# Kernel tuning notes

Measured on AMD Instinct MI355X. Metric: run time of the kernel, lower is better.

The kernel has to match this reference:

```python
import jax, jax.numpy as jnp
import numpy as np

N = 50000          # nodes
E_RAND = 800000    # random edges (self-loops appended -> total 850000)
F_IN = 256         # features_num
H = 128            # hidden
HEADS = 4          # headslayers
C = 40             # num_class
OUTDIM = H + HEADS * H + H  # 768, cat of [x_lin, conv1, conv2]
LRELU = 0.01       # F.leaky_relu default slope
ATT_SLOPE = 0.2    # PyG GATConv negative_slope
BN_EPS = 1e-5


def setup_inputs() -> dict:
    key = jax.random.key(0)
    ks = jax.random.split(key, 20)
    src = jax.random.randint(ks[0], (E_RAND,), 0, N)
    dst = jax.random.randint(ks[1], (E_RAND,), 0, N)
    loops = jnp.arange(N, dtype=src.dtype)
    edge_index = jnp.stack([jnp.concatenate([src, loops]),
                            jnp.concatenate([dst, loops])], axis=0)
    g = lambda k, shape, fan: jax.random.normal(k, shape, jnp.float32) * (1.0 / np.sqrt(fan))
    return {
        "x": jax.random.normal(ks[2], (N, F_IN), jnp.float32),
        "edge_index": edge_index,
        # first_lin
        "fw_W": g(ks[3], (F_IN, H), F_IN), "fw_b": jnp.zeros((H,), jnp.float32),
        # conv1: GATConv(H, H, heads=HEADS)
        "c1_W": g(ks[4], (H, HEADS * H), H),
        "c1_as": g(ks[5], (HEADS, H), H), "c1_ad": g(ks[6], (HEADS, H), H),
        "c1_b": jnp.zeros((HEADS * H,), jnp.float32),
        # conv2: GATConv(HEADS*H, H, heads=1)
        "c2_W": g(ks[7], (HEADS * H, H), HEADS * H),
        "c2_as": g(ks[8], (1, H), H), "c2_ad": g(ks[9], (1, H), H),
        "c2_b": jnp.zeros((H,), jnp.float32),
        # batchnorms (training-mode batch stats)
        "bn1_g": jnp.ones((H,), jnp.float32), "bn1_b": jnp.zeros((H,), jnp.float32),
        "bn2_g": jnp.ones((HEADS * H,), jnp.float32), "bn2_b": jnp.zeros((HEADS * H,), jnp.float32),
        "bn3_g": jnp.ones((H,), jnp.float32), "bn3_b": jnp.zeros((H,), jnp.float32),
        # lin2
        "l2_W": g(ks[10], (OUTDIM, C), OUTDIM), "l2_b": jnp.zeros((C,), jnp.float32),
    }


def _batchnorm(x, gamma, beta):
    mu = jnp.mean(x, axis=0)
    var = jnp.mean(jnp.square(x - mu), axis=0)  # biased, as torch BN training
    return (x - mu) * (gamma / jnp.sqrt(var + BN_EPS)) + beta


def _gat_conv(x, edge_index, W, a_src, a_dst, bias, heads, out_dim):
    src, dst = edge_index[0], edge_index[1]
    h = (x @ W).reshape(-1, heads, out_dim)            # [N, heads, out]
    alpha_s = jnp.sum(h * a_src, axis=-1)              # [N, heads]
    alpha_d = jnp.sum(h * a_dst, axis=-1)              # [N, heads]
    e = alpha_s[src] + alpha_d[dst]                    # [E, heads]
    e = jnp.where(e >= 0, e, ATT_SLOPE * e)            # leaky_relu(0.2)
    # segment softmax over incoming edges of each dst node
    emax = jax.ops.segment_max(e, dst, num_segments=N)
    e = jnp.exp(e - emax[dst])
    denom = jax.ops.segment_sum(e, dst, num_segments=N)
    alpha = e / (denom[dst] + 1e-16)                   # [E, heads]
    msg = h[src] * alpha[:, :, None]                   # [E, heads, out]
    out = jax.ops.segment_sum(msg, dst, num_segments=N)
    return out.reshape(-1, heads * out_dim) + bias


def _lrelu(x):
    return jnp.where(x >= 0, x, LRELU * x)


def reference(x, edge_index, fw_W, fw_b, c1_W, c1_as, c1_ad, c1_b,
              c2_W, c2_as, c2_ad, c2_b, bn1_g, bn1_b, bn2_g, bn2_b,
              bn3_g, bn3_b, l2_W, l2_b):
    h = _lrelu(x @ fw_W + fw_b)
    h = _batchnorm(h, bn1_g, bn1_b)
    feats = [h]
    h = _lrelu(_gat_conv(h, edge_index, c1_W, c1_as, c1_ad, c1_b, HEADS, H))
    h = _batchnorm(h, bn2_g, bn2_b)
    feats.append(h)
    h = _lrelu(_gat_conv(h, edge_index, c2_W, c2_as, c2_ad, c2_b, 1, H))
    h = _batchnorm(h, bn3_g, bn3_b)
    feats.append(h)
    z = jnp.concatenate(feats, axis=1) @ l2_W + l2_b
    return jax.nn.log_softmax(z, axis=-1)
```

## Files before the change

kernel.cpp:

```cpp
#include <hip/hip_runtime.h>

#define INF_F __builtin_inff()

typedef unsigned short u16;
typedef __attribute__((ext_vector_type(8))) short s16x8;
typedef __attribute__((ext_vector_type(4))) float f32x4;

union U8 { uint4 q; s16x8 v; };

__device__ __forceinline__ float b2f(u16 u) {
    union { unsigned int i; float f; } v; v.i = ((unsigned int)u) << 16; return v.f;
}
__device__ __forceinline__ u16 f2b(float f) {
    union { float f; unsigned int i; } v; v.f = f;
    unsigned int r = (v.i + 0x7FFFu + ((v.i >> 16) & 1u)) >> 16;
    return (u16)r;
}
__device__ __forceinline__ void bf2x(unsigned int p, float& lo, float& hi) {
    union { unsigned int i; float f; } a, b;
    a.i = p << 16; b.i = p & 0xFFFF0000u;
    lo = a.f; hi = b.f;
}
__device__ __forceinline__ unsigned int packbf(float lo, float hi) {
    return (unsigned int)f2b(lo) | ((unsigned int)f2b(hi) << 16);
}

__device__ __forceinline__ void pack_one(const float* __restrict__ W, int K, int N,
                                         int Npad, u16* __restrict__ pb, int idx)
{
    int k = idx / Npad, n = idx - k * Npad;
    float v = (n < N) ? W[(size_t)k * N + n] : 0.f;
    int K5 = K >> 5;
    size_t o = ((size_t)(n >> 4) * K5 + (k >> 5)) * 512
             + ((size_t)((k >> 3) & 3)) * 128 + (n & 15) * 8 + (k & 7);
    pb[o] = f2b(v);
}

__launch_bounds__(256)
__global__ void k_prep(const float* __restrict__ fw_W, const float* __restrict__ c1_W,
                       const float* __restrict__ c2_W, const float* __restrict__ l2_W,
                       u16* __restrict__ pb_l1, u16* __restrict__ pb_c1,
                       u16* __restrict__ pb_c2, u16* __restrict__ pb_f,
                       const int* __restrict__ dst, int E, int* __restrict__ counts)
{
    int idx = blockIdx.x * 256 + threadIdx.x;
    if (idx < 32768) { pack_one(fw_W, 256, 128, 128, pb_l1, idx); return; }
    idx -= 32768;
    if (idx < 65536) { pack_one(c1_W, 128, 512, 512, pb_c1, idx); return; }
    idx -= 65536;
    if (idx < 65536) { pack_one(c2_W, 512, 128, 128, pb_c2, idx); return; }
    idx -= 65536;
    if (idx < 49152) { pack_one(l2_W, 768, 40, 64, pb_f, idx); return; }
    idx -= 49152;
    if (idx < E) atomicAdd(&counts[dst[idx]], 1);
}

__launch_bounds__(256)
__global__ void k_l1sc(const float* __restrict__ x, const u16* __restrict__ pb,
                       u16* __restrict__ h1, int M, const float* __restrict__ bias,
                       int mb2, const int* __restrict__ ei, int E,
                       const int* __restrict__ rowstart, int* __restrict__ fill,
                       int* __restrict__ csr)
{
    if ((int)blockIdx.x >= mb2) {
        int e = ((int)blockIdx.x - mb2) * 256 + threadIdx.x;
        if (e < E) {
            int s = ei[e], d = ei[E + e];
            int pos = rowstart[d] + atomicAdd(&fill[d], 1);
            csr[pos] = s;
        }
        return;
    }
    const int tid = threadIdx.x;
    const int w = tid >> 6, l = tid & 63;
    const int lo = l & 15, hi = l >> 4;
    const int row0 = blockIdx.x * 128 + w * 32;
    if (row0 >= M) return;

    f32x4 acc[8][2];
    #pragma unroll
    for (int i = 0; i < 8; ++i)
        #pragma unroll
        for (int s = 0; s < 2; ++s) acc[i][s] = (f32x4){0.f, 0.f, 0.f, 0.f};

    int arow[2];
    #pragma unroll
    for (int s = 0; s < 2; ++s) {
        int r = row0 + s * 16 + lo;
        arow[s] = r < M ? r : M - 1;
    }

    for (int k5 = 0; k5 < 8; ++k5) {
        const int ak = k5 * 32 + hi * 8;
        s16x8 af[2];
        #pragma unroll
        for (int s = 0; s < 2; ++s) {
            const float* A = x + (size_t)arow[s] * 256 + ak;
            float4 v0 = *reinterpret_cast<const float4*>(A);
            float4 v1 = *reinterpret_cast<const float4*>(A + 4);
            U8 au;
            au.q.x = packbf(v0.x, v0.y); au.q.y = packbf(v0.z, v0.w);
            au.q.z = packbf(v1.x, v1.y); au.q.w = packbf(v1.z, v1.w);
            af[s] = au.v;
        }
        #pragma unroll
        for (int cb = 0; cb < 8; ++cb) {
            s16x8 bf = *reinterpret_cast<const s16x8*>(pb + ((size_t)cb * 8 + k5) * 512 + l * 8);
            acc[cb][0] = __builtin_amdgcn_mfma_f32_16x16x32_bf16(af[0], bf, acc[cb][0], 0, 0, 0);
            acc[cb][1] = __builtin_amdgcn_mfma_f32_16x16x32_bf16(af[1], bf, acc[cb][1], 0, 0, 0);
        }
    }

    #pragma unroll
    for (int cb = 0; cb < 8; ++cb) {
        int col = cb * 16 + lo;
        #pragma unroll
        for (int s = 0; s < 2; ++s) {
            #pragma unroll
            for (int p = 0; p < 4; ++p) {
                int r = row0 + s * 16 + hi * 4 + p;
                if (r < M) {
                    float v = acc[cb][s][p] + bias[col];
                    v = v >= 0.f ? v : 0.01f * v;
                    h1[(size_t)r * 128 + col] = f2b(v);
                }
            }
        }
    }
}

template<int NFRAG, bool BN_A, int HEADS_PB>
__launch_bounds__(256)
__global__ void k_mgemm(const u16* __restrict__ Av, int lda, int K,
                        const u16* __restrict__ pb,
                        u16* __restrict__ C, int ldc, int M,
                        const float* __restrict__ scale, const float* __restrict__ shift,
                        const float* __restrict__ aw_s, const float* __restrict__ aw_d,
                        float* __restrict__ as_o, float* __restrict__ ad_o, int nheads)
{
    const int tid = threadIdx.x;
    const int w = tid >> 6, l = tid & 63;
    const int lo = l & 15, hi = l >> 4;
    const int row0 = blockIdx.y * 128 + w * 32;
    if (row0 >= M) return;
    const int cb0 = blockIdx.x * NFRAG;
    const int K5 = K >> 5;

    f32x4 acc[NFRAG][2];
    #pragma unroll
    for (int i = 0; i < NFRAG; ++i)
        #pragma unroll
        for (int s = 0; s < 2; ++s) acc[i][s] = (f32x4){0.f, 0.f, 0.f, 0.f};

    int arow[2];
    #pragma unroll
    for (int s = 0; s < 2; ++s) {
        int r = row0 + s * 16 + lo;
        arow[s] = r < M ? r : M - 1;
    }

    for (int k5 = 0; k5 < K5; ++k5) {
        const int ak = k5 * 32 + hi * 8;
        s16x8 af[2];
        #pragma unroll
        for (int s = 0; s < 2; ++s) {
            uint4 q = *reinterpret_cast<const uint4*>(Av + (size_t)arow[s] * lda + ak);
            float x[8];
            bf2x(q.x, x[0], x[1]); bf2x(q.y, x[2], x[3]);
            bf2x(q.z, x[4], x[5]); bf2x(q.w, x[6], x[7]);
            if (BN_A) {
                #pragma unroll
                for (int j = 0; j < 8; ++j) x[j] = fmaf(x[j], scale[ak + j], shift[ak + j]);
            }
            U8 au;
            au.q.x = packbf(x[0], x[1]); au.q.y = packbf(x[2], x[3]);
            au.q.z = packbf(x[4], x[5]); au.q.w = packbf(x[6], x[7]);
            af[s] = au.v;
        }
        #pragma unroll
        for (int cb = 0; cb < NFRAG; ++cb) {
            s16x8 bf = *reinterpret_cast<const s16x8*>(
                pb + ((size_t)(cb0 + cb) * K5 + k5) * 512 + l * 8);
            acc[cb][0] = __builtin_amdgcn_mfma_f32_16x16x32_bf16(af[0], bf, acc[cb][0], 0, 0, 0);
            acc[cb][1] = __builtin_amdgcn_mfma_f32_16x16x32_bf16(af[1], bf, acc[cb][1], 0, 0, 0);
        }
    }

    #pragma unroll
    for (int cb = 0; cb < NFRAG; ++cb) {
        int col = (cb0 + cb) * 16 + lo;
        #pragma unroll
        for (int s = 0; s < 2; ++s) {
            #pragma unroll
            for (int p = 0; p < 4; ++p) {
                int r = row0 + s * 16 + hi * 4 + p;
                if (r < M) C[(size_t)r * ldc + col] = f2b(acc[cb][s][p]);
            }
        }
    }

    if (HEADS_PB > 0) {
        const int h = (cb0 >> 3);
        #pragma unroll
        for (int s = 0; s < 2; ++s) {
            float ps[4] = {0.f,0.f,0.f,0.f}, pd[4] = {0.f,0.f,0.f,0.f};
            #pragma unroll
            for (int cb = 0; cb < NFRAG; ++cb) {
                int col = (cb0 + cb) * 16 + lo;
                float ws = aw_s[col], wd = aw_d[col];
                #pragma unroll
                for (int p = 0; p < 4; ++p) {
                    ps[p] = fmaf(acc[cb][s][p], ws, ps[p]);
                    pd[p] = fmaf(acc[cb][s][p], wd, pd[p]);
                }
            }
            #pragma unroll
            for (int m = 1; m < 16; m <<= 1) {
                #pragma unroll
                for (int p = 0; p < 4; ++p) {
                    ps[p] += __shfl_xor(ps[p], m, 64);
                    pd[p] += __shfl_xor(pd[p], m, 64);
                }
            }
            if (lo == 0) {
                #pragma unroll
                for (int p = 0; p < 4; ++p) {
                    int r = row0 + s * 16 + hi * 4 + p;
                    if (r < M) {
                        as_o[(size_t)r * nheads + h] = ps[p];
                        ad_o[(size_t)r * nheads + h] = pd[p];
                    }
                }
            }
        }
    }
}

__launch_bounds__(256)
__global__ void k_mfinal(const u16* __restrict__ h1, const u16* __restrict__ h2,
                         const u16* __restrict__ h3,
                         const float* __restrict__ scale, const float* __restrict__ shift,
                         const u16* __restrict__ pb, const float* __restrict__ bias,
                         float* __restrict__ out, int M)
{
    const int tid = threadIdx.x;
    const int w = tid >> 6, l = tid & 63;
    const int lo = l & 15, hi = l >> 4;
    const int row0 = blockIdx.x * 128 + w * 32;
    if (row0 >= M) return;
    const int K5 = 24;

    f32x4 acc[4][2];
    #pragma unroll
    for (int i = 0; i < 4; ++i)
        #pragma unroll
        for (int s = 0; s < 2; ++s) acc[i][s] = (f32x4){0.f, 0.f, 0.f, 0.f};

    int arow[2];
    #pragma unroll
    for (int s = 0; s < 2; ++s) {
        int r = row0 + s * 16 + lo;
        arow[s] = r < M ? r : M - 1;
    }

    for (int k5 = 0; k5 < K5; ++k5) {
        const int kk = k5 * 32 + hi * 8;
        const u16* src; int ld, offk;
        if (kk < 128)      { src = h1; ld = 128; offk = kk; }
        else if (kk < 640) { src = h2; ld = 512; offk = kk - 128; }
        else               { src = h3; ld = 128; offk = kk - 640; }
        s16x8 af[2];
        #pragma unroll
        for (int s = 0; s < 2; ++s) {
            uint4 q = *reinterpret_cast<const uint4*>(src + (size_t)arow[s] * ld + offk);
            float x[8];
            bf2x(q.x, x[0], x[1]); bf2x(q.y, x[2], x[3]);
            bf2x(q.z, x[4], x[5]); bf2x(q.w, x[6], x[7]);
            #pragma unroll
            for (int j = 0; j < 8; ++j) x[j] = fmaf(x[j], scale[kk + j], shift[kk + j]);
            U8 au;
            au.q.x = packbf(x[0], x[1]); au.q.y = packbf(x[2], x[3]);
            au.q.z = packbf(x[4], x[5]); au.q.w = packbf(x[6], x[7]);
            af[s] = au.v;
        }
        #pragma unroll
        for (int cb = 0; cb < 4; ++cb) {
            s16x8 bf = *reinterpret_cast<const s16x8*>(pb + ((size_t)cb * K5 + k5) * 512 + l * 8);
            acc[cb][0] = __builtin_amdgcn_mfma_f32_16x16x32_bf16(af[0], bf, acc[cb][0], 0, 0, 0);
            acc[cb][1] = __builtin_amdgcn_mfma_f32_16x16x32_bf16(af[1], bf, acc[cb][1], 0, 0, 0);
        }
    }

    #pragma unroll
    for (int s = 0; s < 2; ++s) {
        #pragma unroll
        for (int p = 0; p < 4; ++p) {
            int r = row0 + s * 16 + hi * 4 + p;
            float z0 = acc[0][s][p] + bias[lo];
            float z1 = acc[1][s][p] + bias[16 + lo];
            float z2 = -INF_F;
            if (lo < 8) z2 = acc[2][s][p] + bias[32 + lo];
            float mx = fmaxf(fmaxf(z0, z1), z2);
            #pragma unroll
            for (int m = 1; m < 16; m <<= 1) mx = fmaxf(mx, __shfl_xor(mx, m, 64));
            float se = __expf(z0 - mx) + __expf(z1 - mx) + ((lo < 8) ? __expf(z2 - mx) : 0.f);
            #pragma unroll
            for (int m = 1; m < 16; m <<= 1) se += __shfl_xor(se, m, 64);
            float lse = mx + __logf(se);
            if (r < M) {
                out[(size_t)r * 40 + lo]      = z0 - lse;
                out[(size_t)r * 40 + 16 + lo] = z1 - lse;
                if (lo < 8) out[(size_t)r * 40 + 32 + lo] = z2 - lse;
            }
        }
    }
}

__launch_bounds__(256)
__global__ void k_colstats(const u16* __restrict__ X, int M, int C,
                           float* __restrict__ psum, float* __restrict__ psq)
{
    const int CG  = C >> 3;
    const int RPI = 256 / CG;
    const int tid = threadIdx.x;
    const int cg  = tid & (CG - 1);
    const int ro  = tid / CG;
    const int nb  = gridDim.x;
    const int rows_chunk = (M + nb - 1) / nb;
    const int r0 = blockIdx.x * rows_chunk;
    const int r1 = min(M, r0 + rows_chunk);

    float s[8] = {}, q[8] = {};
    for (int r = r0 + ro; r < r1; r += RPI) {
        uint4 u = *reinterpret_cast<const uint4*>(X + (size_t)r * C + cg * 8);
        float x[8];
        bf2x(u.x, x[0], x[1]); bf2x(u.y, x[2], x[3]);
        bf2x(u.z, x[4], x[5]); bf2x(u.w, x[6], x[7]);
        #pragma unroll
        for (int j = 0; j < 8; ++j) { s[j] += x[j]; q[j] = fmaf(x[j], x[j], q[j]); }
    }

    __shared__ float lsum[8][256];
    __shared__ float lsq [8][256];
    #pragma unroll
    for (int j = 0; j < 8; ++j) { lsum[j][tid] = s[j]; lsq[j][tid] = q[j]; }
    __syncthreads();

    if (tid < CG) {
        #pragma unroll
        for (int j = 0; j < 8; ++j) {
            float ss = 0.f, qq = 0.f;
            for (int o = 0; o < RPI; ++o) {
                ss += lsum[j][o * CG + tid];
                qq += lsq [j][o * CG + tid];
            }
            psum[(size_t)blockIdx.x * C + tid * 8 + j] = ss;
            psq [(size_t)blockIdx.x * C + tid * 8 + j] = qq;
        }
    }
}

__launch_bounds__(256)
__global__ void k_colred(const float* __restrict__ psum, const float* __restrict__ psq,
                         const float* __restrict__ g, const float* __restrict__ b,
                         int nb, int M, int C,
                         float* __restrict__ scale, float* __restrict__ shift)
{
    int c = blockIdx.x * 4 + (threadIdx.x >> 6);
    int lane = threadIdx.x & 63;
    if (c >= C) return;
    float s = 0.f, q = 0.f;
    for (int l = lane; l < nb; l += 64) {
        s += psum[(size_t)l * C + c];
        q += psq [(size_t)l * C + c];
    }
    #pragma unroll
    for (int off = 32; off; off >>= 1) {
        s += __shfl_xor(s, off, 64);
        q += __shfl_xor(q, off, 64);
    }
    if (lane == 0) {
        float mu  = s / (float)M;
        float var = q / (float)M - mu * mu;
        float sc  = g[c] * rsqrtf(var + 1e-5f);
        scale[c] = sc;
        shift[c] = b[c] - mu * sc;
    }
}

__launch_bounds__(256)
__global__ void k_scan1(const int* __restrict__ counts, int n,
                        int* __restrict__ rowstart, int* __restrict__ tilesum,
                        int* __restrict__ fill)
{
    const int tid = threadIdx.x;
    const int lane = tid & 63, w = tid >> 6;
    const int i0 = blockIdx.x * 1024 + tid * 4;
    int v0 = 0, v1 = 0, v2 = 0, v3 = 0;
    if (i0 + 3 < n) {
        int4 q = *reinterpret_cast<const int4*>(counts + i0);
        v0 = q.x; v1 = q.y; v2 = q.z; v3 = q.w;
    } else if (i0 < n) {
        v0 = counts[i0];
        if (i0 + 1 < n) v1 = counts[i0 + 1];
        if (i0 + 2 < n) v2 = counts[i0 + 2];
    }
    if (i0 < n) {
        int4 z = make_int4(0, 0, 0, 0);
        if (i0 + 3 < n) *reinterpret_cast<int4*>(fill + i0) = z;
        else {
            fill[i0] = 0;
            if (i0 + 1 < n) fill[i0 + 1] = 0;
            if (i0 + 2 < n) fill[i0 + 2] = 0;
        }
    }
    int s1 = v0 + v1, s2 = s1 + v2, s3 = s2 + v3;
    int x = s3;
    #pragma unroll
    for (int off = 1; off < 64; off <<= 1) {
        int t = __shfl_up(x, off, 64);
        if (lane >= off) x += t;
    }
    __shared__ int wsum[4];
    if (lane == 63) wsum[w] = x;
    __syncthreads();
    int woff = 0;
    #pragma unroll
    for (int i = 0; i < 4; ++i)
        if (i < w) woff += wsum[i];
    int excl = woff + x - s3;
    if (i0 + 0 < n) rowstart[i0 + 1] = excl + v0;
    if (i0 + 1 < n) rowstart[i0 + 2] = excl + s1;
    if (i0 + 2 < n) rowstart[i0 + 3] = excl + s2;
    if (i0 + 3 < n) rowstart[i0 + 4] = excl + s3;
    if (tid == 255) tilesum[blockIdx.x] = wsum[0] + wsum[1] + wsum[2] + wsum[3];
}

__launch_bounds__(256)
__global__ void k_scan3(int* __restrict__ rowstart, const int* __restrict__ tilesum, int n)
{
    const int tile = (int)((blockIdx.x * 256) >> 10);
    __shared__ int s_off;
    if (threadIdx.x < 64) {
        int lane = threadIdx.x;
        int v = (lane < tile) ? tilesum[lane] : 0;
        #pragma unroll
        for (int m = 1; m < 64; m <<= 1) v += __shfl_xor(v, m, 64);
        if (lane == 0) s_off = v;
    }
    __syncthreads();
    int i = blockIdx.x * 256 + threadIdx.x;
    if (i < n) rowstart[i + 1] += s_off;
    if (blockIdx.x == 0 && threadIdx.x == 0) rowstart[0] = 0;
}

__launch_bounds__(256)
__global__ void k_gat_agg_h4(const u16* __restrict__ hp,
                             const float* __restrict__ as_, const float* __restrict__ ad_,
                             const int* __restrict__ rowstart, const int* __restrict__ csr,
                             const float* __restrict__ bias, u16* __restrict__ out, int Nn)
{
    int d = (int)((blockIdx.x * (size_t)blockDim.x + threadIdx.x) >> 6);
    int lane = threadIdx.x & 63;
    if (d >= Nn) return;
    const int h = lane >> 4;
    const int li = lane & 15;
    const int dim = li * 8;
    int e0 = rowstart[d], e1 = rowstart[d + 1];
    float adv = ad_[(size_t)d * 4 + h];

    float mx = -INF_F;
    for (int j = e0 + li; j < e1; j += 16) {
        int s = csr[j];
        float e = as_[(size_t)s * 4 + h] + adv;
        e = e >= 0.f ? e : 0.2f * e;
        mx = fmaxf(mx, e);
    }
    #pragma unroll
    for (int m = 1; m < 16; m <<= 1) mx = fmaxf(mx, __shfl_xor(mx, m, 64));

    float lsum = 0.f;
    float acc[8] = {};

    #define F4(J, A, U) { int jj = min((J), e1 - 1); int s_ = csr[jj];                \
        A = as_[(size_t)s_ * 4 + h];                                                  \
        U = *reinterpret_cast<const uint4*>(hp + ((size_t)s_ * 4 + h) * 128 + dim); }
    #define C4(A, U) { float e_ = A + adv; e_ = e_ >= 0.f ? e_ : 0.2f * e_;           \
        float w_ = __expf(e_ - mx); lsum += w_;                                       \
        float x_[8];                                                                  \
        bf2x(U.x, x_[0], x_[1]); bf2x(U.y, x_[2], x_[3]);                             \
        bf2x(U.z, x_[4], x_[5]); bf2x(U.w, x_[6], x_[7]);                             \
        _Pragma("unroll")                                                             \
        for (int t_ = 0; t_ < 8; ++t_) acc[t_] = fmaf(x_[t_], w_, acc[t_]); }

    float a0, a1, a2, a3, a4, a5, a6, a7;
    uint4 u0, u1, u2, u3, u4, u5, u6, u7;
    F4(e0 + 0, a0, u0); F4(e0 + 1, a1, u1); F4(e0 + 2, a2, u2); F4(e0 + 3, a3, u3);
    F4(e0 + 4, a4, u4); F4(e0 + 5, a5, u5); F4(e0 + 6, a6, u6); F4(e0 + 7, a7, u7);

    int j = e0;
    for (; j + 3 < e1; j += 4) {
        C4(a0, u0); C4(a1, u1); C4(a2, u2); C4(a3, u3);
        a0 = a4; u0 = u4; a1 = a5; u1 = u5; a2 = a6; u2 = u6; a3 = a7; u3 = u7;
        F4(j + 8, a4, u4); F4(j + 9, a5, u5); F4(j + 10, a6, u6); F4(j + 11, a7, u7);
    }
    if (j < e1)     C4(a0, u0);
    if (j + 1 < e1) C4(a1, u1);
    if (j + 2 < e1) C4(a2, u2);
    #undef F4
    #undef C4

    float inv = 1.f / (lsum + 1e-16f);
    const int ob = h * 128 + dim;
    float v[8];
    #pragma unroll
    for (int t = 0; t < 8; ++t) {
        float z = acc[t] * inv + bias[ob + t];
        v[t] = z >= 0.f ? z : 0.01f * z;
    }
    uint4 o;
    o.x = packbf(v[0], v[1]); o.y = packbf(v[2], v[3]);
    o.z = packbf(v[4], v[5]); o.w = packbf(v[6], v[7]);
    *reinterpret_cast<uint4*>(out + (size_t)d * 512 + ob) = o;
}

__launch_bounds__(256)
__global__ void k_gat_agg_h1(const u16* __restrict__ hp,
                             const float* __restrict__ as_, const float* __restrict__ ad_,
                             const int* __restrict__ rowstart, const int* __restrict__ csr,
                             const float* __restrict__ bias, u16* __restrict__ out, int Nn)
{
    const int lane = threadIdx.x & 63;
    const int half = lane >> 5;
    const int sl = lane & 31;
    const int wave = (int)((blockIdx.x * (size_t)blockDim.x + threadIdx.x) >> 6);
    const int d = wave * 2 + half;
    if (wave * 2 >= Nn) return;
    const bool act = d < Nn;
    const int dc = act ? d : (Nn - 1);
    const int dim = sl * 4;
    int e0 = rowstart[dc], e1 = rowstart[dc + 1];
    int len = e1 - e0;
    float adv = ad_[dc];

    float mx = -INF_F;
    for (int j = e0 + sl; j < e1; j += 32) {
        int s = csr[j];
        float e = as_[s] + adv;
        e = e >= 0.f ? e : 0.2f * e;
        mx = fmaxf(mx, e);
    }
    #pragma unroll
    for (int m = 1; m < 32; m <<= 1) mx = fmaxf(mx, __shfl_xor(mx, m, 32));

    int maxlen = max(len, __shfl_xor(len, 32, 64));

    float lsum = 0.f;
    float acc[4] = {};

    #define F1(JR, A, U) { int jj = e0 + min((JR), len - 1); int s_ = csr[jj];        \
        A = as_[s_];                                                                  \
        U = *reinterpret_cast<const uint2*>(hp + (size_t)s_ * 128 + dim); }
    #define C1(JR, A, U) { float e_ = A + adv; e_ = e_ >= 0.f ? e_ : 0.2f * e_;       \
        float w_ = ((JR) < len) ? __expf(e_ - mx) : 0.f;                              \
        float x0_, x1_, x2_, x3_; bf2x(U.x, x0_, x1_); bf2x(U.y, x2_, x3_);           \
        lsum += w_;                                                                   \
        acc[0] = fmaf(x0_, w_, acc[0]); acc[1] = fmaf(x1_, w_, acc[1]);               \
        acc[2] = fmaf(x2_, w_, acc[2]); acc[3] = fmaf(x3_, w_, acc[3]); }

    float a0, a1, a2, a3, a4, a5, a6, a7;
    uint2 u0, u1, u2, u3, u4, u5, u6, u7;
    F1(0, a0, u0); F1(1, a1, u1); F1(2, a2, u2); F1(3, a3, u3);
    F1(4, a4, u4); F1(5, a5, u5); F1(6, a6, u6); F1(7, a7, u7);

    int jr = 0;
    for (; jr + 3 < maxlen; jr += 4) {
        C1(jr + 0, a0, u0); C1(jr + 1, a1, u1); C1(jr + 2, a2, u2); C1(jr + 3, a3, u3);
        a0 = a4; u0 = u4; a1 = a5; u1 = u5; a2 = a6; u2 = u6; a3 = a7; u3 = u7;
        F1(jr + 8, a4, u4); F1(jr + 9, a5, u5); F1(jr + 10, a6, u6); F1(jr + 11, a7, u7);
    }
    if (jr < maxlen)     C1(jr + 0, a0, u0);
    if (jr + 1 < maxlen) C1(jr + 1, a1, u1);
    if (jr + 2 < maxlen) C1(jr + 2, a2, u2);
    #undef F1
    #undef C1

    float inv = 1.f / (lsum + 1e-16f);
    float v0 = acc[0] * inv + bias[dim];
    float v1 = acc[1] * inv + bias[dim + 1];
    float v2 = acc[2] * inv + bias[dim + 2];
    float v3 = acc[3] * inv + bias[dim + 3];
    v0 = v0 >= 0.f ? v0 : 0.01f * v0;
    v1 = v1 >= 0.f ? v1 : 0.01f * v1;
    v2 = v2 >= 0.f ? v2 : 0.01f * v2;
    v3 = v3 >= 0.f ? v3 : 0.01f * v3;
    if (act) {
        uint2 o;
        o.x = packbf(v0, v1);
        o.y = packbf(v2, v3);
        *reinterpret_cast<uint2*>(out + (size_t)d * 128 + dim) = o;
    }
}

extern "C" void kernel_launch(void* const* d_in, const int* in_sizes, int n_in,
                              void* d_out, int out_size, void* d_ws, size_t ws_size,
                              hipStream_t stream)
{
    const float* x     = (const float*)d_in[0];
    const int*   ei    = (const int*)  d_in[1];
    const float* fw_W  = (const float*)d_in[2];
    const float* fw_b  = (const float*)d_in[3];
    const float* c1_W  = (const float*)d_in[4];
    const float* c1_as = (const float*)d_in[5];
    const float* c1_ad = (const float*)d_in[6];
    const float* c1_b  = (const float*)d_in[7];
    const float* c2_W  = (const float*)d_in[8];
    const float* c2_as = (const float*)d_in[9];
    const float* c2_ad = (const float*)d_in[10];
    const float* c2_b  = (const float*)d_in[11];
    const float* bn1_g = (const float*)d_in[12];
    const float* bn1_b = (const float*)d_in[13];
    const float* bn2_g = (const float*)d_in[14];
    const float* bn2_b = (const float*)d_in[15];
    const float* bn3_g = (const float*)d_in[16];
    const float* bn3_b = (const float*)d_in[17];
    const float* l2_W  = (const float*)d_in[18];
    const float* l2_b  = (const float*)d_in[19];
    float* out = (float*)d_out;

    const int N = in_sizes[0] / 256;
    const int E = in_sizes[1] / 2;
    const int NB = 256;

    char* base = (char*)d_ws;
    size_t off = 0;
    auto alloc = [&](size_t bytes) -> void* {
        void* p = (void*)(base + off);
        off = (off + bytes + 255) & ~(size_t)255;
        return p;
    };
    int*   counts = (int*)  alloc((size_t)N * 4);
    size_t zero_bytes = off;
    const int SCB = (N + 1023) / 1024;
    int*   fill     = (int*)  alloc((size_t)N * 4);
    float* as1      = (float*)alloc((size_t)N * 4 * 4);
    float* ad1      = (float*)alloc((size_t)N * 4 * 4);
    float* as2      = (float*)alloc((size_t)N * 4);
    float* ad2      = (float*)alloc((size_t)N * 4);
    float* psum     = (float*)alloc((size_t)NB * 512 * 4);
    float* psq      = (float*)alloc((size_t)NB * 512 * 4);
    int*   rowstart = (int*)  alloc((size_t)(N + 1) * 4);
    int*   tilesum  = (int*)  alloc((size_t)SCB * 4);
    int*   csr      = (int*)  alloc((size_t)E * 4);
    float* scale768 = (float*)alloc(768 * 4);
    float* shift768 = (float*)alloc(768 * 4);
    u16*   pb_l1    = (u16*)  alloc((size_t)256 * 128 * 2);
    u16*   pb_c1    = (u16*)  alloc((size_t)128 * 512 * 2);
    u16*   pb_c2    = (u16*)  alloc((size_t)512 * 128 * 2);
    u16*   pb_f     = (u16*)  alloc((size_t)768 * 64 * 2);
    u16*   h1       = (u16*)  alloc((size_t)N * 128 * 2);
    u16*   h2       = (u16*)  alloc((size_t)N * 512 * 2);
    u16*   hp1      = (u16*)  alloc((size_t)N * 512 * 2);
    u16*   hp2      = hp1;
    u16*   h3       = hp1 + (size_t)N * 128;
    (void)ws_size; (void)n_in; (void)out_size;

    const int mb2 = (N + 127) / 128;
    const int scb = (E + 255) / 256;
    const int wave_blocks = (int)(((size_t)N * 64 + 255) / 256);
    const int h1_wave_blocks = (int)((((size_t)N + 1) / 2 * 64 + 255) / 256);
    const int PK = 32768 + 65536 + 65536 + 49152;

    hipMemsetAsync(base, 0, zero_bytes, stream);

    k_prep<<<(PK + E + 255) / 256, 256, 0, stream>>>(
        fw_W, c1_W, c2_W, l2_W, pb_l1, pb_c1, pb_c2, pb_f, ei + E, E, counts);

    k_scan1<<<SCB, 256, 0, stream>>>(counts, N, rowstart, tilesum, fill);
    k_scan3<<<(N + 255) / 256, 256, 0, stream>>>(rowstart, tilesum, N);

    k_l1sc<<<mb2 + scb, 256, 0, stream>>>(
        x, pb_l1, h1, N, fw_b, mb2, ei, E, rowstart, fill, csr);

    k_colstats<<<NB, 256, 0, stream>>>(h1, N, 128, psum, psq);
    k_colred<<<(128 + 3) / 4, 256, 0, stream>>>(psum, psq, bn1_g, bn1_b, NB, N, 128,
                                                scale768, shift768);

    k_mgemm<8, true, 1><<<dim3(4, mb2), 256, 0, stream>>>(
        h1, 128, 128, pb_c1, hp1, 512, N, scale768, shift768,
        c1_as, c1_ad, as1, ad1, 4);
    k_gat_agg_h4<<<wave_blocks, 256, 0, stream>>>(
        hp1, as1, ad1, rowstart, csr, c1_b, h2, N);

    k_colstats<<<NB, 256, 0, stream>>>(h2, N, 512, psum, psq);
    k_colred<<<(512 + 3) / 4, 256, 0, stream>>>(psum, psq, bn2_g, bn2_b, NB, N, 512,
                                                scale768 + 128, shift768 + 128);

    k_mgemm<8, true, 1><<<dim3(1, mb2), 256, 0, stream>>>(
        h2, 512, 512, pb_c2, hp2, 128, N, scale768 + 128, shift768 + 128,
        c2_as, c2_ad, as2, ad2, 1);
    k_gat_agg_h1<<<h1_wave_blocks, 256, 0, stream>>>(
        hp2, as2, ad2, rowstart, csr, c2_b, h3, N);

    k_colstats<<<NB, 256, 0, stream>>>(h3, N, 128, psum, psq);
    k_colred<<<(128 + 3) / 4, 256, 0, stream>>>(psum, psq, bn3_g, bn3_b, NB, N, 128,
                                                scale768 + 640, shift768 + 640);

    k_mfinal<<<mb2, 256, 0, stream>>>(h1, h2, h3, scale768, shift768, pb_f, l2_b, out, N);
}
```

Baseline: 412.0 us.

## Merge CSR build stages with layer-1 GEMM and BN stats into shared launches

Rearranges the front of the pipeline so independent work shares a launch. The first-layer GEMM runs alongside scan1, scan3 alongside the BN1 column stats, and the edge scatter alongside the BN1 column reduction. This cuts the launch count from five to three and overlaps small latency-bound kernels with bigger ones. The scatter also now handles four edges per thread with int4 loads. The risk is that heterogeneous blocks in one grid may load-balance poorly, and the larger shared-memory footprint of the combined kernels can lower occupancy.

```diff
diff --git a/kernel.cpp b/kernel.cpp
--- a/kernel.cpp
+++ b/kernel.cpp
@@ -55,26 +55,14 @@
     if (idx < E) atomicAdd(&counts[dst[idx]], 1);
 }
 
-__launch_bounds__(256)
-__global__ void k_l1sc(const float* __restrict__ x, const u16* __restrict__ pb,
-                       u16* __restrict__ h1, int M, const float* __restrict__ bias,
-                       int mb2, const int* __restrict__ ei, int E,
-                       const int* __restrict__ rowstart, int* __restrict__ fill,
-                       int* __restrict__ csr)
-{
-    if ((int)blockIdx.x >= mb2) {
-        int e = ((int)blockIdx.x - mb2) * 256 + threadIdx.x;
-        if (e < E) {
-            int s = ei[e], d = ei[E + e];
-            int pos = rowstart[d] + atomicAdd(&fill[d], 1);
-            csr[pos] = s;
-        }
-        return;
-    }
+__device__ void dev_l1gemm(const float* __restrict__ x, const u16* __restrict__ pb,
+                           u16* __restrict__ h1, int M, const float* __restrict__ bias,
+                           int bid)
+{
     const int tid = threadIdx.x;
     const int w = tid >> 6, l = tid & 63;
     const int lo = l & 15, hi = l >> 4;
-    const int row0 = blockIdx.x * 128 + w * 32;
+    const int row0 = bid * 128 + w * 32;
     if (row0 >= M) return;
 
     f32x4 acc[8][2];
@@ -127,6 +115,210 @@
             }
         }
     }
+}
+
+__device__ void dev_scan1(const int* __restrict__ counts, int n,
+                          int* __restrict__ rowstart, int* __restrict__ tilesum,
+                          int* __restrict__ fill, int bid)
+{
+    const int tid = threadIdx.x;
+    const int lane = tid & 63, w = tid >> 6;
+    const int i0 = bid * 1024 + tid * 4;
+    int v0 = 0, v1 = 0, v2 = 0, v3 = 0;
+    if (i0 + 3 < n) {
+        int4 q = *reinterpret_cast<const int4*>(counts + i0);
+        v0 = q.x; v1 = q.y; v2 = q.z; v3 = q.w;
+    } else if (i0 < n) {
+        v0 = counts[i0];
+        if (i0 + 1 < n) v1 = counts[i0 + 1];
+        if (i0 + 2 < n) v2 = counts[i0 + 2];
+    }
+    if (i0 < n) {
+        int4 z = make_int4(0, 0, 0, 0);
+        if (i0 + 3 < n) *reinterpret_cast<int4*>(fill + i0) = z;
+        else {
+            fill[i0] = 0;
+            if (i0 + 1 < n) fill[i0 + 1] = 0;
+            if (i0 + 2 < n) fill[i0 + 2] = 0;
+        }
+    }
+    int s1 = v0 + v1, s2 = s1 + v2, s3 = s2 + v3;
+    int x = s3;
+    #pragma unroll
+    for (int off = 1; off < 64; off <<= 1) {
+        int t = __shfl_up(x, off, 64);
+        if (lane >= off) x += t;
+    }
+    __shared__ int wsum[4];
+    if (lane == 63) wsum[w] = x;
+    __syncthreads();
+    int woff = 0;
+    #pragma unroll
+    for (int i = 0; i < 4; ++i)
+        if (i < w) woff += wsum[i];
+    int excl = woff + x - s3;
+    if (i0 + 0 < n) rowstart[i0 + 1] = excl + v0;
+    if (i0 + 1 < n) rowstart[i0 + 2] = excl + s1;
+    if (i0 + 2 < n) rowstart[i0 + 3] = excl + s2;
+    if (i0 + 3 < n) rowstart[i0 + 4] = excl + s3;
+    if (tid == 255) tilesum[bid] = wsum[0] + wsum[1] + wsum[2] + wsum[3];
+}
+
+__device__ void dev_scan3(int* __restrict__ rowstart, const int* __restrict__ tilesum,
+                          int n, int bid)
+{
+    const int tile = (bid * 256) >> 10;
+    __shared__ int s_off;
+    if (threadIdx.x < 64) {
+        int lane = threadIdx.x;
+        int v = (lane < tile) ? tilesum[lane] : 0;
+        #pragma unroll
+        for (int m = 1; m < 64; m <<= 1) v += __shfl_xor(v, m, 64);
+        if (lane == 0) s_off = v;
+    }
+    __syncthreads();
+    int i = bid * 256 + threadIdx.x;
+    if (i < n) rowstart[i + 1] += s_off;
+    if (bid == 0 && threadIdx.x == 0) rowstart[0] = 0;
+}
+
+__device__ void dev_colstats(const u16* __restrict__ X, int M, int C,
+                             float* __restrict__ psum, float* __restrict__ psq,
+                             int bid, int nb)
+{
+    const int CG  = C >> 3;
+    const int RPI = 256 / CG;
+    const int tid = threadIdx.x;
+    const int cg  = tid & (CG - 1);
+    const int ro  = tid / CG;
+    const int rows_chunk = (M + nb - 1) / nb;
+    const int r0 = bid * rows_chunk;
+    const int r1 = min(M, r0 + rows_chunk);
+
+    float s[8] = {}, q[8] = {};
+    for (int r = r0 + ro; r < r1; r += RPI) {
+        uint4 u = *reinterpret_cast<const uint4*>(X + (size_t)r * C + cg * 8);
+        float x[8];
+        bf2x(u.x, x[0], x[1]); bf2x(u.y, x[2], x[3]);
+        bf2x(u.z, x[4], x[5]); bf2x(u.w, x[6], x[7]);
+        #pragma unroll
+        for (int j = 0; j < 8; ++j) { s[j] += x[j]; q[j] = fmaf(x[j], x[j], q[j]); }
+    }
+
+    __shared__ float lsum[8][256];
+    __shared__ float lsq [8][256];
+    #pragma unroll
+    for (int j = 0; j < 8; ++j) { lsum[j][tid] = s[j]; lsq[j][tid] = q[j]; }
+    __syncthreads();
+
+    if (tid < CG) {
+        #pragma unroll
+        for (int j = 0; j < 8; ++j) {
+            float ss = 0.f, qq = 0.f;
+            for (int o = 0; o < RPI; ++o) {
+                ss += lsum[j][o * CG + tid];
+                qq += lsq [j][o * CG + tid];
+            }
+            psum[(size_t)bid * C + tid * 8 + j] = ss;
+            psq [(size_t)bid * C + tid * 8 + j] = qq;
+        }
+    }
+}
+
+__device__ void dev_colred(const float* __restrict__ psum, const float* __restrict__ psq,
+                           const float* __restrict__ g, const float* __restrict__ b,
+                           int nb, int M, int C,
+                           float* __restrict__ scale, float* __restrict__ shift, int bid)
+{
+    int c = bid * 4 + ((int)threadIdx.x >> 6);
+    int lane = threadIdx.x & 63;
+    if (c >= C) return;
+    float s = 0.f, q = 0.f;
+    for (int l = lane; l < nb; l += 64) {
+        s += psum[(size_t)l * C + c];
+        q += psq [(size_t)l * C + c];
+    }
+    #pragma unroll
+    for (int off = 32; off; off >>= 1) {
+        s += __shfl_xor(s, off, 64);
+        q += __shfl_xor(q, off, 64);
+    }
+    if (lane == 0) {
+        float mu  = s / (float)M;
+        float var = q / (float)M - mu * mu;
+        float sc  = g[c] * rsqrtf(var + 1e-5f);
+        scale[c] = sc;
+        shift[c] = b[c] - mu * sc;
+    }
+}
+
+__device__ void dev_scatter4(const int* __restrict__ ei, int E,
+                             const int* __restrict__ rowstart,
+                             int* __restrict__ fill, int* __restrict__ csr, int bid)
+{
+    int e0 = (bid * 256 + (int)threadIdx.x) * 4;
+    if (e0 >= E) return;
+    if (e0 + 3 < E) {
+        int4 s4 = *reinterpret_cast<const int4*>(ei + e0);
+        int4 d4 = *reinterpret_cast<const int4*>(ei + E + e0);
+        int p0 = rowstart[d4.x] + atomicAdd(&fill[d4.x], 1); csr[p0] = s4.x;
+        int p1 = rowstart[d4.y] + atomicAdd(&fill[d4.y], 1); csr[p1] = s4.y;
+        int p2 = rowstart[d4.z] + atomicAdd(&fill[d4.z], 1); csr[p2] = s4.z;
+        int p3 = rowstart[d4.w] + atomicAdd(&fill[d4.w], 1); csr[p3] = s4.w;
+    } else {
+        for (int e = e0; e < E; ++e) {
+            int s = ei[e], d = ei[E + e];
+            int pos = rowstart[d] + atomicAdd(&fill[d], 1);
+            csr[pos] = s;
+        }
+    }
+}
+
+__launch_bounds__(256)
+__global__ void kA(const float* __restrict__ x, const u16* __restrict__ pb_l1,
+                   u16* __restrict__ h1, int M, const float* __restrict__ fw_b, int mb2,
+                   const int* __restrict__ counts, int n,
+                   int* __restrict__ rowstart, int* __restrict__ tilesum,
+                   int* __restrict__ fill)
+{
+    if ((int)blockIdx.x < mb2) dev_l1gemm(x, pb_l1, h1, M, fw_b, blockIdx.x);
+    else                       dev_scan1(counts, n, rowstart, tilesum, fill, blockIdx.x - mb2);
+}
+
+__launch_bounds__(256)
+__global__ void kB(int* __restrict__ rowstart, const int* __restrict__ tilesum, int n,
+                   int nscan3, const u16* __restrict__ h1, int M,
+                   float* __restrict__ psum, float* __restrict__ psq, int nb)
+{
+    if ((int)blockIdx.x < nscan3) dev_scan3(rowstart, tilesum, n, blockIdx.x);
+    else                          dev_colstats(h1, M, 128, psum, psq, blockIdx.x - nscan3, nb);
+}
+
+__launch_bounds__(256)
+__global__ void kC(const int* __restrict__ ei, int E, const int* __restrict__ rowstart,
+                   int* __restrict__ fill, int* __restrict__ csr, int nscat,
+                   const float* __restrict__ psum, const float* __restrict__ psq,
+                   const float* __restrict__ g, const float* __restrict__ b,
+                   int nb, int M, float* __restrict__ scale, float* __restrict__ shift)
+{
+    if ((int)blockIdx.x < nscat) dev_scatter4(ei, E, rowstart, fill, csr, blockIdx.x);
+    else dev_colred(psum, psq, g, b, nb, M, 128, scale, shift, blockIdx.x - nscat);
+}
+
+__launch_bounds__(256)
+__global__ void k_colstats(const u16* __restrict__ X, int M, int C,
+                           float* __restrict__ psum, float* __restrict__ psq)
+{
+    dev_colstats(X, M, C, psum, psq, blockIdx.x, gridDim.x);
+}
+
+__launch_bounds__(256)
+__global__ void k_colred(const float* __restrict__ psum, const float* __restrict__ psq,
+                         const float* __restrict__ g, const float* __restrict__ b,
+                         int nb, int M, int C,
+                         float* __restrict__ scale, float* __restrict__ shift)
+{
+    dev_colred(psum, psq, g, b, nb, M, C, scale, shift, blockIdx.x);
 }
 
 template<int NFRAG, bool BN_A, int HEADS_PB>
@@ -314,144 +506,6 @@
             }
         }
     }
-}
-
-__launch_bounds__(256)
-__global__ void k_colstats(const u16* __restrict__ X, int M, int C,
-                           float* __restrict__ psum, float* __restrict__ psq)
-{
-    const int CG  = C >> 3;
-    const int RPI = 256 / CG;
-    const int tid = threadIdx.x;
-    const int cg  = tid & (CG - 1);
-    const int ro  = tid / CG;
-    const int nb  = gridDim.x;
-    const int rows_chunk = (M + nb - 1) / nb;
-    const int r0 = blockIdx.x * rows_chunk;
-    const int r1 = min(M, r0 + rows_chunk);
-
-    float s[8] = {}, q[8] = {};
-    for (int r = r0 + ro; r < r1; r += RPI) {
-        uint4 u = *reinterpret_cast<const uint4*>(X + (size_t)r * C + cg * 8);
-        float x[8];
-        bf2x(u.x, x[0], x[1]); bf2x(u.y, x[2], x[3]);
-        bf2x(u.z, x[4], x[5]); bf2x(u.w, x[6], x[7]);
-        #pragma unroll
-        for (int j = 0; j < 8; ++j) { s[j] += x[j]; q[j] = fmaf(x[j], x[j], q[j]); }
-    }
-
-    __shared__ float lsum[8][256];
-    __shared__ float lsq [8][256];
-    #pragma unroll
-    for (int j = 0; j < 8; ++j) { lsum[j][tid] = s[j]; lsq[j][tid] = q[j]; }
-    __syncthreads();
-
-    if (tid < CG) {
-        #pragma unroll
-        for (int j = 0; j < 8; ++j) {
-            float ss = 0.f, qq = 0.f;
-            for (int o = 0; o < RPI; ++o) {
-                ss += lsum[j][o * CG + tid];
-                qq += lsq [j][o * CG + tid];
-            }
-            psum[(size_t)blockIdx.x * C + tid * 8 + j] = ss;
-            psq [(size_t)blockIdx.x * C + tid * 8 + j] = qq;
-        }
-    }
-}
-
-__launch_bounds__(256)
-__global__ void k_colred(const float* __restrict__ psum, const float* __restrict__ psq,
-                         const float* __restrict__ g, const float* __restrict__ b,
-                         int nb, int M, int C,
-                         float* __restrict__ scale, float* __restrict__ shift)
-{
-    int c = blockIdx.x * 4 + (threadIdx.x >> 6);
-    int lane = threadIdx.x & 63;
-    if (c >= C) return;
-    float s = 0.f, q = 0.f;
-    for (int l = lane; l < nb; l += 64) {
-        s += psum[(size_t)l * C + c];
-        q += psq [(size_t)l * C + c];
-    }
-    #pragma unroll
-    for (int off = 32; off; off >>= 1) {
-        s += __shfl_xor(s, off, 64);
-        q += __shfl_xor(q, off, 64);
-    }
-    if (lane == 0) {
-        float mu  = s / (float)M;
-        float var = q / (float)M - mu * mu;
-        float sc  = g[c] * rsqrtf(var + 1e-5f);
-        scale[c] = sc;
-        shift[c] = b[c] - mu * sc;
-    }
-}
-
-__launch_bounds__(256)
-__global__ void k_scan1(const int* __restrict__ counts, int n,
-                        int* __restrict__ rowstart, int* __restrict__ tilesum,
-                        int* __restrict__ fill)
-{
-    const int tid = threadIdx.x;
-    const int lane = tid & 63, w = tid >> 6;
-    const int i0 = blockIdx.x * 1024 + tid * 4;
-    int v0 = 0, v1 = 0, v2 = 0, v3 = 0;
-    if (i0 + 3 < n) {
-        int4 q = *reinterpret_cast<const int4*>(counts + i0);
-        v0 = q.x; v1 = q.y; v2 = q.z; v3 = q.w;
-    } else if (i0 < n) {
-        v0 = counts[i0];
-        if (i0 + 1 < n) v1 = counts[i0 + 1];
-        if (i0 + 2 < n) v2 = counts[i0 + 2];
-    }
-    if (i0 < n) {
-        int4 z = make_int4(0, 0, 0, 0);
-        if (i0 + 3 < n) *reinterpret_cast<int4*>(fill + i0) = z;
-        else {
-            fill[i0] = 0;
-            if (i0 + 1 < n) fill[i0 + 1] = 0;
-            if (i0 + 2 < n) fill[i0 + 2] = 0;
-        }
-    }
-    int s1 = v0 + v1, s2 = s1 + v2, s3 = s2 + v3;
-    int x = s3;
-    #pragma unroll
-    for (int off = 1; off < 64; off <<= 1) {
-        int t = __shfl_up(x, off, 64);
-        if (lane >= off) x += t;
-    }
-    __shared__ int wsum[4];
-    if (lane == 63) wsum[w] = x;
-    __syncthreads();
-    int woff = 0;
-    #pragma unroll
-    for (int i = 0; i < 4; ++i)
-        if (i < w) woff += wsum[i];
-    int excl = woff + x - s3;
-    if (i0 + 0 < n) rowstart[i0 + 1] = excl + v0;
-    if (i0 + 1 < n) rowstart[i0 + 2] = excl + s1;
-    if (i0 + 2 < n) rowstart[i0 + 3] = excl + s2;
-    if (i0 + 3 < n) rowstart[i0 + 4] = excl + s3;
-    if (tid == 255) tilesum[blockIdx.x] = wsum[0] + wsum[1] + wsum[2] + wsum[3];
-}
-
-__launch_bounds__(256)
-__global__ void k_scan3(int* __restrict__ rowstart, const int* __restrict__ tilesum, int n)
-{
-    const int tile = (int)((blockIdx.x * 256) >> 10);
-    __shared__ int s_off;
-    if (threadIdx.x < 64) {
-        int lane = threadIdx.x;
-        int v = (lane < tile) ? tilesum[lane] : 0;
-        #pragma unroll
-        for (int m = 1; m < 64; m <<= 1) v += __shfl_xor(v, m, 64);
-        if (lane == 0) s_off = v;
-    }
-    __syncthreads();
-    int i = blockIdx.x * 256 + threadIdx.x;
-    if (i < n) rowstart[i + 1] += s_off;
-    if (blockIdx.x == 0 && threadIdx.x == 0) rowstart[0] = 0;
 }
 
 __launch_bounds__(256)
@@ -666,7 +720,8 @@
     (void)ws_size; (void)n_in; (void)out_size;
 
     const int mb2 = (N + 127) / 128;
-    const int scb = (E + 255) / 256;
+    const int nscan3 = (N + 255) / 256;
+    const int nscat4 = (E + 1023) / 1024;
     const int wave_blocks = (int)(((size_t)N * 64 + 255) / 256);
     const int h1_wave_blocks = (int)((((size_t)N + 1) / 2 * 64 + 255) / 256);
     const int PK = 32768 + 65536 + 65536 + 49152;
@@ -676,15 +731,15 @@
     k_prep<<<(PK + E + 255) / 256, 256, 0, stream>>>(
         fw_W, c1_W, c2_W, l2_W, pb_l1, pb_c1, pb_c2, pb_f, ei + E, E, counts);
 
-    k_scan1<<<SCB, 256, 0, stream>>>(counts, N, rowstart, tilesum, fill);
-    k_scan3<<<(N + 255) / 256, 256, 0, stream>>>(rowstart, tilesum, N);
-
-    k_l1sc<<<mb2 + scb, 256, 0, stream>>>(
-        x, pb_l1, h1, N, fw_b, mb2, ei, E, rowstart, fill, csr);
-
-    k_colstats<<<NB, 256, 0, stream>>>(h1, N, 128, psum, psq);
-    k_colred<<<(128 + 3) / 4, 256, 0, stream>>>(psum, psq, bn1_g, bn1_b, NB, N, 128,
-                                                scale768, shift768);
+    kA<<<mb2 + SCB, 256, 0, stream>>>(
+        x, pb_l1, h1, N, fw_b, mb2, counts, N, rowstart, tilesum, fill);
+
+    kB<<<nscan3 + NB, 256, 0, stream>>>(
+        rowstart, tilesum, N, nscan3, h1, N, psum, psq, NB);
+
+    kC<<<nscat4 + (128 + 3) / 4, 256, 0, stream>>>(
+        ei, E, rowstart, fill, csr, nscat4,
+        psum, psq, bn1_g, bn1_b, NB, N, scale768, shift768);
 
     k_mgemm<8, true, 1><<<dim3(4, mb2), 256, 0, stream>>>(
         h1, 128, 128, pb_c1, hp1, 512, N, scale768, shift768,
```

After: 420.9 us. 1.02x slower.
